# Performance work log

Hardware: AMD Instinct MI355X
Metric: run time of the kernel (lower is better)

Reference implementation:

```python
import jax, jax.numpy as jnp
import numpy as np

B, S, D, VOCAB = 8, 32, 256, 50257
N = 4 * 64          # n_devices * neurons_per_device
K = max(N // 5, 8)  # top-k active neurons = 51


def _make_edges():
    # mimics the torch init loop: 4*N random (src,dst) draws, keep src!=dst, dedup, preserve order
    rng = np.random.default_rng(0)
    s = rng.integers(0, N, 4 * N)
    d = rng.integers(0, N, 4 * N)
    seen, es, ed = set(), [], []
    for a, b in zip(s.tolist(), d.tolist()):
        if a != b and (a, b) not in seen:
            seen.add((a, b)); es.append(a); ed.append(b)
    return np.asarray(es, np.int32), np.asarray(ed, np.int32)


def setup_inputs() -> dict:
    key = jax.random.key(0)
    ks = jax.random.split(key, 12)
    es, ed = _make_edges()
    E = es.shape[0]
    f32 = jnp.float32
    return {
        "input_ids": jax.random.randint(ks[0], (B, S), 0, VOCAB),
        "embed":     jax.random.normal(ks[1], (VOCAB, D), f32) * 0.02,
        "pos_embed": jax.random.normal(ks[2], (S, D), f32) * 0.02,
        "router_W":  jax.random.normal(ks[3], (N, D), f32) * 0.02,
        "router_b":  jnp.zeros((N,), f32),
        "fc_W":      jax.random.normal(ks[4], (N, D, D), f32) * 0.02,
        "fc_b":      jnp.zeros((N, D), f32),
        "gate_W":    jax.random.normal(ks[5], (N, D), f32) * 0.02,
        "gate_b":    jnp.zeros((N,), f32),
        "conn_W":    jax.random.normal(ks[6], (E, D, D), f32) * 0.02,
        "ln_g":      jnp.ones((D,), f32),
        "ln_b":      jnp.zeros((D,), f32),
        "out_W":     jax.random.normal(ks[7], (VOCAB, D), f32) * 0.02,
        "out_b":     jnp.zeros((VOCAB,), f32),
        "edge_src":  jnp.asarray(es),
        "edge_dst":  jnp.asarray(ed),
    }


def _forward(input_ids, embed, pos_embed, router_W, router_b, fc_W, fc_b,
             gate_W, gate_b, conn_W, ln_g, ln_b, out_W, out_b, edge_src, edge_dst):
    x = embed[input_ids] + pos_embed[None, :, :]  # [B,S,D]

    def propagate(xt):  # xt: [B,D] -> [B,D]
        scores = xt @ router_W.T + router_b                  # [B,N]
        vals, idx = jax.lax.top_k(scores, K)                 # [B,K]
        active = idx[0]                                      # batch-elem-0 picks the active set (as in torch code)
        w = jax.nn.softmax(vals, axis=-1)                    # [B,K]
        # hop 0: active neurons applied to routed input
        h = jnp.einsum('bd,kod->kbo', xt, fc_W[active]) + fc_b[active][:, None, :]
        g = jax.nn.sigmoid(jnp.einsum('bd,kd->kb', xt, gate_W[active]) + gate_b[active][:, None])
        states = jax.nn.gelu(h, approximate=False) * g[:, :, None] * w.T[:, :, None]  # [K,B,D]
        # edge pass: only edges with both endpoints active contribute
        member = jnp.zeros((N,), bool).at[active].set(True)
        pos = jnp.zeros((N,), jnp.int32).at[active].set(jnp.arange(K, dtype=jnp.int32))
        emask = (member[edge_src] & member[edge_dst]).astype(xt.dtype)               # [E]
        sig = jnp.einsum('ebd,eod->ebo', states[pos[edge_src]], conn_W)              # [E,B,D]
        hh = jnp.einsum('ebd,eod->ebo', sig, fc_W[edge_dst]) + fc_b[edge_dst][:, None, :]
        gg = jax.nn.sigmoid(jnp.einsum('ebd,ed->eb', sig, gate_W[edge_dst]) + gate_b[edge_dst][:, None])
        act = jax.nn.gelu(hh, approximate=False) * gg[:, :, None] * emask[:, None, None]
        nxt = jax.ops.segment_sum(act, pos[edge_dst], num_segments=K)                # [K,B,D]
        return (states + 0.5 * nxt).mean(axis=0)                                     # [B,D]

    out = jax.vmap(propagate, in_axes=1, out_axes=1)(x)      # [B,S,D]
    mu = out.mean(-1, keepdims=True)
    var = ((out - mu) ** 2).mean(-1, keepdims=True)
    out = (out - mu) * jax.lax.rsqrt(var + 1e-5) * ln_g + ln_b
    return out @ out_W.T + out_b                             # [B,S,VOCAB]


def reference(input_ids, embed, pos_embed, router_W, router_b, fc_W, fc_b,
              gate_W, gate_b, conn_W, ln_g, ln_b, out_W, out_b, edge_src, edge_dst):
    return _forward(input_ids, embed, pos_embed, router_W, router_b, fc_W, fc_b,
                    gate_W, gate_b, conn_W, ln_g, ln_b, out_W, out_b, edge_src, edge_dst)
```

## Files before the change

kernel.cpp:

```cpp
#include <hip/hip_runtime.h>
#include <math.h>

#define B_ 8
#define S_ 32
#define D_ 256
#define N_ 256
#define K_ 51
#define V_ 50257

__device__ __forceinline__ float dot4f(float4 a, float4 b){
  return a.x*b.x + a.y*b.y + a.z*b.z + a.w*b.w;
}
__device__ __forceinline__ float gelu_exact(float x){
  return 0.5f * x * (1.0f + erff(x * 0.70710678118654752440f));
}
__device__ __forceinline__ float sigmoidf_(float x){
  return 1.0f / (1.0f + expf(-x));
}

__global__ __launch_bounds__(256) void k_embed(const int* __restrict__ ids,
    const float* __restrict__ embed, const float* __restrict__ pose,
    float* __restrict__ xt)
{
  int bx = blockIdx.x;
  int t = bx >> 3, b = bx & 7;
  int d = threadIdx.x;
  int id = ids[b * S_ + t];
  xt[(size_t)bx * D_ + d] = embed[(size_t)id * D_ + d] + pose[(size_t)t * D_ + d];
}

__global__ __launch_bounds__(256) void k_router(const float* __restrict__ xt,
    const float* __restrict__ rW, const float* __restrict__ rb,
    float* __restrict__ scores)
{
  int bx = blockIdx.x;
  int tid = threadIdx.x;
  __shared__ float4 xs4[64];
  if (tid < 64) xs4[tid] = ((const float4*)(xt + (size_t)bx * D_))[tid];
  __syncthreads();
  float acc = rb[tid];
  const float4* wp = (const float4*)(rW + (size_t)tid * D_);
  for (int d4 = 0; d4 < 64; d4++){
    float4 w = wp[d4]; float4 x = xs4[d4];
    acc += dot4f(w, x);
  }
  scores[(size_t)bx * N_ + tid] = acc;
}

__global__ __launch_bounds__(256) void k_topk(const float* __restrict__ scores,
    float* __restrict__ wbuf, int* __restrict__ active,
    int* __restrict__ member, int* __restrict__ pos)
{
  int bx = blockIdx.x;
  int t = bx >> 3, b = bx & 7;
  int tid = threadIdx.x;
  __shared__ float sv[256];
  __shared__ int   si[256];
  __shared__ float ex[K_];
  __shared__ float exsum;
  sv[tid] = scores[(size_t)bx * N_ + tid];
  si[tid] = tid;
  for (int kk = 2; kk <= 256; kk <<= 1){
    for (int j = kk >> 1; j > 0; j >>= 1){
      __syncthreads();
      int ixj = tid ^ j;
      if (ixj > tid){
        float va = sv[tid], vb = sv[ixj];
        int   ia = si[tid], ib = si[ixj];
        bool before = (va > vb) || (va == vb && ia < ib);
        bool up = ((tid & kk) == 0);
        if (up != before){
          sv[tid] = vb; sv[ixj] = va;
          si[tid] = ib; si[ixj] = ia;
        }
      }
    }
  }
  __syncthreads();
  float vmax = sv[0];
  if (tid < K_) ex[tid] = expf(sv[tid] - vmax);
  __syncthreads();
  if (tid == 0){
    float s = 0.0f;
    for (int k = 0; k < K_; k++) s += ex[k];
    exsum = s;
  }
  __syncthreads();
  if (tid < K_) wbuf[(size_t)bx * K_ + tid] = ex[tid] / exsum;
  if (b == 0){
    member[t * N_ + tid] = 0;
    pos[t * N_ + tid] = 0;
    __syncthreads();
    if (tid < K_){
      int nn = si[tid];
      active[t * K_ + tid] = nn;
      member[t * N_ + nn] = 1;
      pos[t * N_ + nn] = tid;
    }
  }
}

__global__ __launch_bounds__(256) void k_chunks(const int* __restrict__ esrc,
    const int* __restrict__ edst, const int* __restrict__ member,
    int E, int* __restrict__ ccount, unsigned int* __restrict__ chunks)
{
  int e = blockIdx.x * 256 + threadIdx.x;
  if (e >= E) return;
  int src = esrc[e], dst = edst[e];
  unsigned int mask = 0;
  for (int t = 0; t < S_; t++)
    if (member[t * N_ + src] && member[t * N_ + dst]) mask |= (1u << t);
  while (mask){
    int t0 = __ffs(mask) - 1; mask &= mask - 1;
    unsigned int t1 = 0xFFu;
    if (mask){ t1 = (unsigned int)(__ffs(mask) - 1); mask &= mask - 1; }
    int ci = atomicAdd(ccount, 1);
    chunks[ci] = (unsigned int)e | ((unsigned int)t0 << 16) | (t1 << 24);
  }
}

__global__ __launch_bounds__(256) void k_hop0(const float* __restrict__ xt,
    const float* __restrict__ fcW, const float* __restrict__ fcB,
    const float* __restrict__ gateW, const float* __restrict__ gateB,
    const float* __restrict__ wbuf, const int* __restrict__ active,
    float* __restrict__ states)
{
  int k = blockIdx.x, t = blockIdx.y;
  int tid = threadIdx.x;
  __shared__ float xs[B_ * D_];
  __shared__ float gl[B_];
  __shared__ float wl[B_];
  int n = active[t * K_ + k];
  float4* xs4 = (float4*)xs;
  const float4* xt4 = (const float4*)(xt + (size_t)t * B_ * D_);
  #pragma unroll
  for (int i = 0; i < 2; i++) xs4[tid + i * 256] = xt4[tid + i * 256];
  if (tid < B_) wl[tid] = wbuf[(size_t)(t * B_ + tid) * K_ + k];
  __syncthreads();
  {
    int wave = tid >> 6, lane = tid & 63;
    float4 gw = ((const float4*)(gateW + (size_t)n * D_))[lane];
    float a0 = dot4f(gw, xs4[(wave * 2 + 0) * 64 + lane]);
    float a1 = dot4f(gw, xs4[(wave * 2 + 1) * 64 + lane]);
    for (int s2 = 1; s2 < 64; s2 <<= 1){
      a0 += __shfl_xor(a0, s2, 64);
      a1 += __shfl_xor(a1, s2, 64);
    }
    if (lane == 0){
      float gb = gateB[n];
      gl[wave * 2 + 0] = sigmoidf_(a0 + gb);
      gl[wave * 2 + 1] = sigmoidf_(a1 + gb);
    }
  }
  __syncthreads();
  float acc[B_] = {0,0,0,0,0,0,0,0};
  const float4* wp = (const float4*)(fcW + (size_t)n * D_ * D_ + (size_t)tid * D_);
  for (int d4 = 0; d4 < 64; d4++){
    float4 w = wp[d4];
    #pragma unroll
    for (int b = 0; b < B_; b++) acc[b] += dot4f(w, xs4[b * 64 + d4]);
  }
  float fb = fcB[(size_t)n * D_ + tid];
  #pragma unroll
  for (int b = 0; b < B_; b++){
    float s = gelu_exact(acc[b] + fb) * gl[b] * wl[b];
    states[((size_t)(t * K_ + k) * B_ + b) * D_ + tid] = s;
  }
}

__global__ __launch_bounds__(256) void k_edge3(const float* __restrict__ states,
    const float* __restrict__ connW, const float* __restrict__ fcW,
    const float* __restrict__ fcB, const float* __restrict__ gateW,
    const float* __restrict__ gateB, const int* __restrict__ esrc,
    const int* __restrict__ edst, const int* __restrict__ pos,
    const int* __restrict__ ccount, const unsigned int* __restrict__ chunks,
    float* __restrict__ nxt)
{
  __shared__ float xs[2 * B_ * D_];
  __shared__ float sg[2 * B_ * D_];
  __shared__ float gl[16];
  int nch = *ccount;
  int tid = threadIdx.x;
  float4* xs4 = (float4*)xs;
  float4* sg4 = (float4*)sg;
  for (int it = blockIdx.x; it < nch; it += gridDim.x){
    unsigned int pk = chunks[it];
    int e  = (int)(pk & 0xFFFFu);
    int t0 = (int)((pk >> 16) & 0xFFu);
    int t1 = (int)((pk >> 24) & 0xFFu);
    int nc = (t1 == 0xFF) ? 1 : 2;
    int src = esrc[e], dst = edst[e];
    int ks0 = pos[t0 * N_ + src], kd0 = pos[t0 * N_ + dst];
    {
      const float4* s0 = (const float4*)(states + (size_t)(t0 * K_ + ks0) * B_ * D_);
      xs4[tid] = s0[tid]; xs4[tid + 256] = s0[tid + 256];
      if (nc == 2){
        int ks1 = pos[t1 * N_ + src];
        const float4* s1 = (const float4*)(states + (size_t)(t1 * K_ + ks1) * B_ * D_);
        xs4[tid + 512] = s1[tid]; xs4[tid + 768] = s1[tid + 256];
      }
    }
    __syncthreads();
    {
      const float4* wp = (const float4*)(connW + (size_t)e * D_ * D_ + (size_t)tid * D_);
      if (nc == 2){
        float a0[B_] = {0,0,0,0,0,0,0,0};
        float a1[B_] = {0,0,0,0,0,0,0,0};
        #pragma unroll 16
        for (int d4 = 0; d4 < 64; d4++){
          float4 w = wp[d4];
          #pragma unroll
          for (int b = 0; b < B_; b++){
            a0[b] += dot4f(w, xs4[b * 64 + d4]);
            a1[b] += dot4f(w, xs4[512 + b * 64 + d4]);
          }
        }
        #pragma unroll
        for (int b = 0; b < B_; b++){
          sg[b * D_ + tid] = a0[b];
          sg[2048 + b * D_ + tid] = a1[b];
        }
      } else {
        float a0[B_] = {0,0,0,0,0,0,0,0};
        #pragma unroll 16
        for (int d4 = 0; d4 < 64; d4++){
          float4 w = wp[d4];
          #pragma unroll
          for (int b = 0; b < B_; b++) a0[b] += dot4f(w, xs4[b * 64 + d4]);
        }
        #pragma unroll
        for (int b = 0; b < B_; b++) sg[b * D_ + tid] = a0[b];
      }
    }
    __syncthreads();
    {
      int wv = tid >> 6, ln = tid & 63;
      float4 gw = ((const float4*)(gateW + (size_t)dst * D_))[ln];
      float gb = gateB[dst];
      for (int p = wv; p < 8 * nc; p += 4){
        float a = dot4f(gw, sg4[(p >> 3) * 512 + (p & 7) * 64 + ln]);
        for (int s2 = 1; s2 < 64; s2 <<= 1) a += __shfl_xor(a, s2, 64);
        if (ln == 0) gl[p] = sigmoidf_(a + gb);
      }
    }
    __syncthreads();
    {
      const float4* wq = (const float4*)(fcW + (size_t)dst * D_ * D_ + (size_t)tid * D_);
      float fb = fcB[(size_t)dst * D_ + tid];
      if (nc == 2){
        float b0[B_] = {0,0,0,0,0,0,0,0};
        float b1[B_] = {0,0,0,0,0,0,0,0};
        #pragma unroll 16
        for (int d4 = 0; d4 < 64; d4++){
          float4 w = wq[d4];
          #pragma unroll
          for (int b = 0; b < B_; b++){
            b0[b] += dot4f(w, sg4[b * 64 + d4]);
            b1[b] += dot4f(w, sg4[512 + b * 64 + d4]);
          }
        }
        int kd1 = pos[t1 * N_ + dst];
        float* nx0 = nxt + (size_t)(t0 * K_ + kd0) * B_ * D_;
        float* nx1 = nxt + (size_t)(t1 * K_ + kd1) * B_ * D_;
        #pragma unroll
        for (int b = 0; b < B_; b++){
          atomicAdd(&nx0[b * D_ + tid], gelu_exact(b0[b] + fb) * gl[b]);
          atomicAdd(&nx1[b * D_ + tid], gelu_exact(b1[b] + fb) * gl[8 + b]);
        }
      } else {
        float b0[B_] = {0,0,0,0,0,0,0,0};
        #pragma unroll 16
        for (int d4 = 0; d4 < 64; d4++){
          float4 w = wq[d4];
          #pragma unroll
          for (int b = 0; b < B_; b++) b0[b] += dot4f(w, sg4[b * 64 + d4]);
        }
        float* nx0 = nxt + (size_t)(t0 * K_ + kd0) * B_ * D_;
        #pragma unroll
        for (int b = 0; b < B_; b++)
          atomicAdd(&nx0[b * D_ + tid], gelu_exact(b0[b] + fb) * gl[b]);
      }
    }
    __syncthreads();
  }
}

__global__ __launch_bounds__(256) void k_ln(const float* __restrict__ states,
    const float* __restrict__ nxt, const float* __restrict__ lng,
    const float* __restrict__ lnb, float* __restrict__ normed)
{
  int row = blockIdx.x;
  int b = row >> 5, t = row & 31;
  int d = threadIdx.x;
  float v = 0.0f;
  for (int k = 0; k < K_; k++){
    size_t idx = ((size_t)(t * K_ + k) * B_ + b) * D_ + d;
    v += states[idx] + 0.5f * nxt[idx];
  }
  v /= 51.0f;
  __shared__ float red[256];
  red[d] = v; __syncthreads();
  for (int s = 128; s > 0; s >>= 1){ if (d < s) red[d] += red[d + s]; __syncthreads(); }
  float mu = red[0] * (1.0f / 256.0f);
  __syncthreads();
  float c = v - mu;
  red[d] = c * c; __syncthreads();
  for (int s = 128; s > 0; s >>= 1){ if (d < s) red[d] += red[d + s]; __syncthreads(); }
  float var = red[0] * (1.0f / 256.0f);
  normed[(size_t)row * D_ + d] = c * rsqrtf(var + 1e-5f) * lng[d] + lnb[d];
}

__global__ __launch_bounds__(256) void k_logits(const float* __restrict__ normed,
    const float* __restrict__ outW, const float* __restrict__ outB,
    float* __restrict__ out)
{
  __shared__ float Ws[64][132];
  __shared__ float Xs[64][68];
  int tid = threadIdx.x;
  int vbase = blockIdx.x * 128;
  int rbase = blockIdx.y * 64;
  int cg = tid & 31;
  int rg = tid >> 5;
  float acc[8][4];
  #pragma unroll
  for (int i = 0; i < 8; i++)
    #pragma unroll
    for (int j = 0; j < 4; j++) acc[i][j] = 0.0f;

  for (int kb = 0; kb < 4; kb++){
    if (kb) __syncthreads();
    #pragma unroll
    for (int i = 0; i < 8; i++){
      int idx = tid + i * 256;
      int v = idx >> 4, kq = idx & 15;
      int gv = vbase + v;
      float4 w = make_float4(0.0f, 0.0f, 0.0f, 0.0f);
      if (gv < V_) w = ((const float4*)(outW + (size_t)gv * D_))[kb * 16 + kq];
      Ws[kq * 4 + 0][v] = w.x;
      Ws[kq * 4 + 1][v] = w.y;
      Ws[kq * 4 + 2][v] = w.z;
      Ws[kq * 4 + 3][v] = w.w;
    }
    #pragma unroll
    for (int i = 0; i < 4; i++){
      int idx = tid + i * 256;
      int r = idx >> 4, kq = idx & 15;
      float4 x = ((const float4*)(normed + (size_t)(rbase + r) * D_))[kb * 16 + kq];
      Xs[kq * 4 + 0][r] = x.x;
      Xs[kq * 4 + 1][r] = x.y;
      Xs[kq * 4 + 2][r] = x.z;
      Xs[kq * 4 + 3][r] = x.w;
    }
    __syncthreads();
    #pragma unroll 4
    for (int k = 0; k < 64; k++){
      float4 wv = *(const float4*)&Ws[k][cg * 4];
      float4 x0 = *(const float4*)&Xs[k][rg * 8];
      float4 x1 = *(const float4*)&Xs[k][rg * 8 + 4];
      float xr[8] = {x0.x, x0.y, x0.z, x0.w, x1.x, x1.y, x1.z, x1.w};
      float wc[4] = {wv.x, wv.y, wv.z, wv.w};
      #pragma unroll
      for (int i = 0; i < 8; i++)
        #pragma unroll
        for (int j = 0; j < 4; j++)
          acc[i][j] = fmaf(xr[i], wc[j], acc[i][j]);
    }
  }
  #pragma unroll
  for (int j = 0; j < 4; j++){
    int gc = vbase + cg * 4 + j;
    if (gc < V_){
      float ob = outB[gc];
      #pragma unroll
      for (int i = 0; i < 8; i++)
        out[(size_t)(rbase + rg * 8 + i) * V_ + gc] = acc[i][j] + ob;
    }
  }
}

extern "C" void kernel_launch(void* const* d_in, const int* in_sizes, int n_in,
                              void* d_out, int out_size, void* d_ws, size_t ws_size,
                              hipStream_t stream)
{
  const int*   ids    = (const int*)d_in[0];
  const float* embed  = (const float*)d_in[1];
  const float* pose   = (const float*)d_in[2];
  const float* rW     = (const float*)d_in[3];
  const float* rb     = (const float*)d_in[4];
  const float* fcW    = (const float*)d_in[5];
  const float* fcB    = (const float*)d_in[6];
  const float* gateW  = (const float*)d_in[7];
  const float* gateB  = (const float*)d_in[8];
  const float* connW  = (const float*)d_in[9];
  const float* lng    = (const float*)d_in[10];
  const float* lnb    = (const float*)d_in[11];
  const float* outW   = (const float*)d_in[12];
  const float* outB   = (const float*)d_in[13];
  const int*   esrc   = (const int*)d_in[14];
  const int*   edst   = (const int*)d_in[15];
  int E = in_sizes[14];
  float* out = (float*)d_out;

  char* ws = (char*)d_ws;
  float* xt     = (float*)(ws + 0);
  float* scores = (float*)(ws + 262144);
  unsigned int* chunks = (unsigned int*)(ws + 262144);
  float* wbuf   = (float*)(ws + 524288);
  int*   active = (int*)  (ws + 589824);
  int*   ccount = (int*)  (ws + 596992);
  int*   member = (int*)  (ws + 598016);
  int*   pos    = (int*)  (ws + 630784);
  float* states = (float*)(ws + 663552);
  float* nxt    = (float*)(ws + 14032896);
  float* normed = (float*)(ws + 27402240);

  hipMemsetAsync(nxt, 0, (size_t)3342336 * 4, stream);

  k_embed  <<<dim3(S_ * B_), 256, 0, stream>>>(ids, embed, pose, xt);
  k_router <<<dim3(S_ * B_), 256, 0, stream>>>(xt, rW, rb, scores);
  k_topk   <<<dim3(S_ * B_), 256, 0, stream>>>(scores, wbuf, active, member, pos);
  hipMemsetAsync(ccount, 0, 4, stream);
  k_chunks <<<dim3((E + 255) / 256), 256, 0, stream>>>(esrc, edst, member, E, ccount, chunks);
  k_hop0   <<<dim3(K_, S_), 256, 0, stream>>>(xt, fcW, fcB, gateW, gateB, wbuf, active, states);
  k_edge3  <<<dim3(1024), 256, 0, stream>>>(states, connW, fcW, fcB, gateW, gateB,
                                            esrc, edst, pos, ccount, chunks, nxt);
  k_ln     <<<dim3(B_ * S_), 256, 0, stream>>>(states, nxt, lng, lnb, normed);
  k_logits <<<dim3((V_ + 127) / 128, 4), 256, 0, stream>>>(normed, outW, outB, out);
}
```

Baseline: 795.8 us.

## Group hop0 by neuron across timesteps and tile edge matmuls through shared memory

Hop0 is reorganised so each block handles one neuron for up to four timesteps. The neuron's fc weight is loaded once and reused via a shared-memory-tiled register-blocked GEMM, and the block also zeroes the matching nxt slices, which replaces the big memset. The edge kernel switches from per-thread full-row weight reads to cooperatively staged, transposed weight tiles in shared memory with a 4x4 register-blocked outer product. This cuts redundant global weight traffic and improves coalescing, at the cost of more syncs, more shared memory and an extra small chunk-building kernel.

```diff
diff --git a/kernel.cpp b/kernel.cpp
--- a/kernel.cpp
+++ b/kernel.cpp
@@ -119,52 +119,121 @@
   }
 }
 
+__global__ __launch_bounds__(256) void k_nchunks(const int* __restrict__ member,
+    int* __restrict__ ncount, unsigned int* __restrict__ nchunks)
+{
+  int n = threadIdx.x;
+  unsigned int mask = 0;
+  for (int t = 0; t < S_; t++)
+    if (member[t * N_ + n]) mask |= (1u << t);
+  while (mask){
+    unsigned int t0 = (unsigned int)(__ffs(mask) - 1); mask &= mask - 1;
+    unsigned int t1 = 0x3Fu, t2 = 0x3Fu, t3 = 0x3Fu;
+    if (mask){ t1 = (unsigned int)(__ffs(mask) - 1); mask &= mask - 1; }
+    if (mask){ t2 = (unsigned int)(__ffs(mask) - 1); mask &= mask - 1; }
+    if (mask){ t3 = (unsigned int)(__ffs(mask) - 1); mask &= mask - 1; }
+    int ci = atomicAdd(ncount, 1);
+    nchunks[ci] = (unsigned int)n | (t0 << 8) | (t1 << 14) | (t2 << 20) | (t3 << 26);
+  }
+}
+
 __global__ __launch_bounds__(256) void k_hop0(const float* __restrict__ xt,
     const float* __restrict__ fcW, const float* __restrict__ fcB,
     const float* __restrict__ gateW, const float* __restrict__ gateB,
-    const float* __restrict__ wbuf, const int* __restrict__ active,
-    float* __restrict__ states)
-{
-  int k = blockIdx.x, t = blockIdx.y;
+    const float* __restrict__ wbuf, const int* __restrict__ pos,
+    const int* __restrict__ ncount, const unsigned int* __restrict__ nchunks,
+    float* __restrict__ states, float* __restrict__ nxt)
+{
+  __shared__ float XT[256][36];
+  __shared__ float Ws[32][260];
+  __shared__ float gl[32];
+  int nch = *ncount;
   int tid = threadIdx.x;
-  __shared__ float xs[B_ * D_];
-  __shared__ float gl[B_];
-  __shared__ float wl[B_];
-  int n = active[t * K_ + k];
-  float4* xs4 = (float4*)xs;
-  const float4* xt4 = (const float4*)(xt + (size_t)t * B_ * D_);
-  #pragma unroll
-  for (int i = 0; i < 2; i++) xs4[tid + i * 256] = xt4[tid + i * 256];
-  if (tid < B_) wl[tid] = wbuf[(size_t)(t * B_ + tid) * K_ + k];
-  __syncthreads();
-  {
-    int wave = tid >> 6, lane = tid & 63;
-    float4 gw = ((const float4*)(gateW + (size_t)n * D_))[lane];
-    float a0 = dot4f(gw, xs4[(wave * 2 + 0) * 64 + lane]);
-    float a1 = dot4f(gw, xs4[(wave * 2 + 1) * 64 + lane]);
-    for (int s2 = 1; s2 < 64; s2 <<= 1){
-      a0 += __shfl_xor(a0, s2, 64);
-      a1 += __shfl_xor(a1, s2, 64);
-    }
-    if (lane == 0){
+  int cg = tid & 63;
+  int rg = tid >> 6;
+  for (int it = blockIdx.x; it < nch; it += gridDim.x){
+    __syncthreads();
+    unsigned int pk = nchunks[it];
+    int n = (int)(pk & 255u);
+    int nt = 1 + (((pk >> 14) & 63u) != 63u) + (((pk >> 20) & 63u) != 63u)
+               + (((pk >> 26) & 63u) != 63u);
+    #pragma unroll
+    for (int i = 0; i < 8; i++){
+      int idx = tid + i * 256;
+      int r = idx & 31, kq = idx >> 5;
+      int ti = r >> 3, b = r & 7;
+      float4 v = make_float4(0.0f, 0.0f, 0.0f, 0.0f);
+      if (ti < nt){
+        int t = (int)((pk >> (8 + 6 * ti)) & 63u);
+        v = ((const float4*)(xt + (size_t)(t * 8 + b) * D_))[kq];
+      }
+      XT[kq * 4 + 0][r] = v.x;
+      XT[kq * 4 + 1][r] = v.y;
+      XT[kq * 4 + 2][r] = v.z;
+      XT[kq * 4 + 3][r] = v.w;
+    }
+    if (rg < nt){
+      int t = (int)((pk >> (8 + 6 * rg)) & 63u);
+      float4 gw = ((const float4*)(gateW + (size_t)n * D_))[cg];
       float gb = gateB[n];
-      gl[wave * 2 + 0] = sigmoidf_(a0 + gb);
-      gl[wave * 2 + 1] = sigmoidf_(a1 + gb);
-    }
-  }
-  __syncthreads();
-  float acc[B_] = {0,0,0,0,0,0,0,0};
-  const float4* wp = (const float4*)(fcW + (size_t)n * D_ * D_ + (size_t)tid * D_);
-  for (int d4 = 0; d4 < 64; d4++){
-    float4 w = wp[d4];
-    #pragma unroll
-    for (int b = 0; b < B_; b++) acc[b] += dot4f(w, xs4[b * 64 + d4]);
-  }
-  float fb = fcB[(size_t)n * D_ + tid];
-  #pragma unroll
-  for (int b = 0; b < B_; b++){
-    float s = gelu_exact(acc[b] + fb) * gl[b] * wl[b];
-    states[((size_t)(t * K_ + k) * B_ + b) * D_ + tid] = s;
+      for (int b = 0; b < 8; b++){
+        float a = dot4f(gw, ((const float4*)(xt + (size_t)(t * 8 + b) * D_))[cg]);
+        for (int s2 = 1; s2 < 64; s2 <<= 1) a += __shfl_xor(a, s2, 64);
+        if (cg == 0) gl[rg * 8 + b] = sigmoidf_(a + gb);
+      }
+    }
+    __syncthreads();
+    float acc[8][4];
+    #pragma unroll
+    for (int i = 0; i < 8; i++)
+      #pragma unroll
+      for (int j = 0; j < 4; j++) acc[i][j] = 0.0f;
+    const float4* wsrc = (const float4*)(fcW + (size_t)n * D_ * D_);
+    for (int kb = 0; kb < 8; kb++){
+      if (kb) __syncthreads();
+      #pragma unroll
+      for (int i = 0; i < 8; i++){
+        int idx = tid + i * 256;
+        int o = idx >> 3, q = idx & 7;
+        float4 w = wsrc[(size_t)o * 64 + kb * 8 + q];
+        Ws[q * 4 + 0][o] = w.x;
+        Ws[q * 4 + 1][o] = w.y;
+        Ws[q * 4 + 2][o] = w.z;
+        Ws[q * 4 + 3][o] = w.w;
+      }
+      __syncthreads();
+      #pragma unroll 8
+      for (int kk = 0; kk < 32; kk++){
+        float4 w = *(const float4*)&Ws[kk][cg * 4];
+        float4 xa = *(const float4*)&XT[kb * 32 + kk][rg * 8];
+        float4 xb = *(const float4*)&XT[kb * 32 + kk][rg * 8 + 4];
+        float xr[8] = {xa.x, xa.y, xa.z, xa.w, xb.x, xb.y, xb.z, xb.w};
+        float wc[4] = {w.x, w.y, w.z, w.w};
+        #pragma unroll
+        for (int i = 0; i < 8; i++)
+          #pragma unroll
+          for (int j = 0; j < 4; j++)
+            acc[i][j] = fmaf(xr[i], wc[j], acc[i][j]);
+      }
+    }
+    if (rg < nt){
+      int t = (int)((pk >> (8 + 6 * rg)) & 63u);
+      int kpos = pos[t * N_ + n];
+      float4 fb = ((const float4*)(fcB + (size_t)n * D_))[cg];
+      #pragma unroll
+      for (int b = 0; b < 8; b++){
+        float w_ = wbuf[(size_t)(t * 8 + b) * K_ + kpos];
+        float g_ = gl[rg * 8 + b];
+        float4 o4;
+        o4.x = gelu_exact(acc[b][0] + fb.x) * g_ * w_;
+        o4.y = gelu_exact(acc[b][1] + fb.y) * g_ * w_;
+        o4.z = gelu_exact(acc[b][2] + fb.z) * g_ * w_;
+        o4.w = gelu_exact(acc[b][3] + fb.w) * g_ * w_;
+        size_t base = ((size_t)(t * K_ + kpos) * 8 + b) * D_ + cg * 4;
+        *(float4*)(states + base) = o4;
+        *(float4*)(nxt + base) = make_float4(0.0f, 0.0f, 0.0f, 0.0f);
+      }
+    }
   }
 }
 
@@ -176,14 +245,16 @@
     const int* __restrict__ ccount, const unsigned int* __restrict__ chunks,
     float* __restrict__ nxt)
 {
-  __shared__ float xs[2 * B_ * D_];
-  __shared__ float sg[2 * B_ * D_];
+  __shared__ float XT[256][20];
+  __shared__ float Ws[32][260];
+  __shared__ float sgl[16][260];
   __shared__ float gl[16];
   int nch = *ccount;
   int tid = threadIdx.x;
-  float4* xs4 = (float4*)xs;
-  float4* sg4 = (float4*)sg;
+  int cg = tid & 63;
+  int rg = tid >> 6;
   for (int it = blockIdx.x; it < nch; it += gridDim.x){
+    __syncthreads();
     unsigned int pk = chunks[it];
     int e  = (int)(pk & 0xFFFFu);
     int t0 = (int)((pk >> 16) & 0xFFu);
@@ -191,97 +262,132 @@
     int nc = (t1 == 0xFF) ? 1 : 2;
     int src = esrc[e], dst = edst[e];
     int ks0 = pos[t0 * N_ + src], kd0 = pos[t0 * N_ + dst];
+    int ks1 = (nc == 2) ? pos[t1 * N_ + src] : 0;
+    int kd1 = (nc == 2) ? pos[t1 * N_ + dst] : 0;
+    #pragma unroll
+    for (int i = 0; i < 4; i++){
+      int idx = tid + i * 256;
+      int r = idx & 15, kq = idx >> 4;
+      int c = r >> 3, b = r & 7;
+      float4 v = make_float4(0.0f, 0.0f, 0.0f, 0.0f);
+      if (c < nc){
+        int t = c ? t1 : t0;
+        int ks = c ? ks1 : ks0;
+        v = ((const float4*)(states + ((size_t)(t * K_ + ks) * 8 + b) * D_))[kq];
+      }
+      XT[kq * 4 + 0][r] = v.x;
+      XT[kq * 4 + 1][r] = v.y;
+      XT[kq * 4 + 2][r] = v.z;
+      XT[kq * 4 + 3][r] = v.w;
+    }
+    __syncthreads();
+    float acc[4][4];
+    #pragma unroll
+    for (int i = 0; i < 4; i++)
+      #pragma unroll
+      for (int j = 0; j < 4; j++) acc[i][j] = 0.0f;
     {
-      const float4* s0 = (const float4*)(states + (size_t)(t0 * K_ + ks0) * B_ * D_);
-      xs4[tid] = s0[tid]; xs4[tid + 256] = s0[tid + 256];
-      if (nc == 2){
-        int ks1 = pos[t1 * N_ + src];
-        const float4* s1 = (const float4*)(states + (size_t)(t1 * K_ + ks1) * B_ * D_);
-        xs4[tid + 512] = s1[tid]; xs4[tid + 768] = s1[tid + 256];
-      }
-    }
-    __syncthreads();
+      const float4* wsrc = (const float4*)(connW + (size_t)e * D_ * D_);
+      for (int kb = 0; kb < 8; kb++){
+        if (kb) __syncthreads();
+        #pragma unroll
+        for (int i = 0; i < 8; i++){
+          int idx = tid + i * 256;
+          int o = idx >> 3, q = idx & 7;
+          float4 w = wsrc[(size_t)o * 64 + kb * 8 + q];
+          Ws[q * 4 + 0][o] = w.x;
+          Ws[q * 4 + 1][o] = w.y;
+          Ws[q * 4 + 2][o] = w.z;
+          Ws[q * 4 + 3][o] = w.w;
+        }
+        __syncthreads();
+        #pragma unroll 8
+        for (int kk = 0; kk < 32; kk++){
+          float4 w = *(const float4*)&Ws[kk][cg * 4];
+          float4 x = *(const float4*)&XT[kb * 32 + kk][rg * 4];
+          float xr[4] = {x.x, x.y, x.z, x.w};
+          float wc[4] = {w.x, w.y, w.z, w.w};
+          #pragma unroll
+          for (int i = 0; i < 4; i++)
+            #pragma unroll
+            for (int j = 0; j < 4; j++)
+              acc[i][j] = fmaf(xr[i], wc[j], acc[i][j]);
+        }
+      }
+    }
+    #pragma unroll
+    for (int i = 0; i < 4; i++)
+      *(float4*)&sgl[rg * 4 + i][cg * 4] = make_float4(acc[i][0], acc[i][1], acc[i][2], acc[i][3]);
+    __syncthreads();
+    #pragma unroll
+    for (int i = 0; i < 4; i++){
+      int idx = tid + i * 256;
+      int r = idx & 15, kq = idx >> 4;
+      float4 v = *(const float4*)&sgl[r][kq * 4];
+      XT[kq * 4 + 0][r] = v.x;
+      XT[kq * 4 + 1][r] = v.y;
+      XT[kq * 4 + 2][r] = v.z;
+      XT[kq * 4 + 3][r] = v.w;
+    }
     {
-      const float4* wp = (const float4*)(connW + (size_t)e * D_ * D_ + (size_t)tid * D_);
-      if (nc == 2){
-        float a0[B_] = {0,0,0,0,0,0,0,0};
-        float a1[B_] = {0,0,0,0,0,0,0,0};
-        #pragma unroll 16
-        for (int d4 = 0; d4 < 64; d4++){
-          float4 w = wp[d4];
+      float4 gw = ((const float4*)(gateW + (size_t)dst * D_))[cg];
+      float gb = gateB[dst];
+      for (int p = rg; p < 8 * nc; p += 4){
+        float a = dot4f(gw, *(const float4*)&sgl[p][cg * 4]);
+        for (int s2 = 1; s2 < 64; s2 <<= 1) a += __shfl_xor(a, s2, 64);
+        if (cg == 0) gl[p] = sigmoidf_(a + gb);
+      }
+    }
+    __syncthreads();
+    #pragma unroll
+    for (int i = 0; i < 4; i++)
+      #pragma unroll
+      for (int j = 0; j < 4; j++) acc[i][j] = 0.0f;
+    {
+      const float4* wsrc = (const float4*)(fcW + (size_t)dst * D_ * D_);
+      for (int kb = 0; kb < 8; kb++){
+        if (kb) __syncthreads();
+        #pragma unroll
+        for (int i = 0; i < 8; i++){
+          int idx = tid + i * 256;
+          int o = idx >> 3, q = idx & 7;
+          float4 w = wsrc[(size_t)o * 64 + kb * 8 + q];
+          Ws[q * 4 + 0][o] = w.x;
+          Ws[q * 4 + 1][o] = w.y;
+          Ws[q * 4 + 2][o] = w.z;
+          Ws[q * 4 + 3][o] = w.w;
+        }
+        __syncthreads();
+        #pragma unroll 8
+        for (int kk = 0; kk < 32; kk++){
+          float4 w = *(const float4*)&Ws[kk][cg * 4];
+          float4 x = *(const float4*)&XT[kb * 32 + kk][rg * 4];
+          float xr[4] = {x.x, x.y, x.z, x.w};
+          float wc[4] = {w.x, w.y, w.z, w.w};
           #pragma unroll
-          for (int b = 0; b < B_; b++){
-            a0[b] += dot4f(w, xs4[b * 64 + d4]);
-            a1[b] += dot4f(w, xs4[512 + b * 64 + d4]);
-          }
+          for (int i = 0; i < 4; i++)
+            #pragma unroll
+            for (int j = 0; j < 4; j++)
+              acc[i][j] = fmaf(xr[i], wc[j], acc[i][j]);
         }
-        #pragma unroll
-        for (int b = 0; b < B_; b++){
-          sg[b * D_ + tid] = a0[b];
-          sg[2048 + b * D_ + tid] = a1[b];
-        }
-      } else {
-        float a0[B_] = {0,0,0,0,0,0,0,0};
-        #pragma unroll 16
-        for (int d4 = 0; d4 < 64; d4++){
-          float4 w = wp[d4];
-          #pragma unroll
-          for (int b = 0; b < B_; b++) a0[b] += dot4f(w, xs4[b * 64 + d4]);
-        }
-        #pragma unroll
-        for (int b = 0; b < B_; b++) sg[b * D_ + tid] = a0[b];
-      }
-    }
-    __syncthreads();
-    {
-      int wv = tid >> 6, ln = tid & 63;
-      float4 gw = ((const float4*)(gateW + (size_t)dst * D_))[ln];
-      float gb = gateB[dst];
-      for (int p = wv; p < 8 * nc; p += 4){
-        float a = dot4f(gw, sg4[(p >> 3) * 512 + (p & 7) * 64 + ln]);
-        for (int s2 = 1; s2 < 64; s2 <<= 1) a += __shfl_xor(a, s2, 64);
-        if (ln == 0) gl[p] = sigmoidf_(a + gb);
-      }
-    }
-    __syncthreads();
-    {
-      const float4* wq = (const float4*)(fcW + (size_t)dst * D_ * D_ + (size_t)tid * D_);
-      float fb = fcB[(size_t)dst * D_ + tid];
-      if (nc == 2){
-        float b0[B_] = {0,0,0,0,0,0,0,0};
-        float b1[B_] = {0,0,0,0,0,0,0,0};
-        #pragma unroll 16
-        for (int d4 = 0; d4 < 64; d4++){
-          float4 w = wq[d4];
-          #pragma unroll
-          for (int b = 0; b < B_; b++){
-            b0[b] += dot4f(w, sg4[b * 64 + d4]);
-            b1[b] += dot4f(w, sg4[512 + b * 64 + d4]);
-          }
-        }
-        int kd1 = pos[t1 * N_ + dst];
-        float* nx0 = nxt + (size_t)(t0 * K_ + kd0) * B_ * D_;
-        float* nx1 = nxt + (size_t)(t1 * K_ + kd1) * B_ * D_;
-        #pragma unroll
-        for (int b = 0; b < B_; b++){
-          atomicAdd(&nx0[b * D_ + tid], gelu_exact(b0[b] + fb) * gl[b]);
-          atomicAdd(&nx1[b * D_ + tid], gelu_exact(b1[b] + fb) * gl[8 + b]);
-        }
-      } else {
-        float b0[B_] = {0,0,0,0,0,0,0,0};
-        #pragma unroll 16
-        for (int d4 = 0; d4 < 64; d4++){
-          float4 w = wq[d4];
-          #pragma unroll
-          for (int b = 0; b < B_; b++) b0[b] += dot4f(w, sg4[b * 64 + d4]);
-        }
-        float* nx0 = nxt + (size_t)(t0 * K_ + kd0) * B_ * D_;
-        #pragma unroll
-        for (int b = 0; b < B_; b++)
-          atomicAdd(&nx0[b * D_ + tid], gelu_exact(b0[b] + fb) * gl[b]);
-      }
-    }
-    __syncthreads();
+      }
+    }
+    float4 fb = ((const float4*)(fcB + (size_t)dst * D_))[cg];
+    #pragma unroll
+    for (int i = 0; i < 4; i++){
+      int m = rg * 4 + i;
+      int c = m >> 3, b = m & 7;
+      if (c < nc){
+        int t = c ? t1 : t0;
+        int kd = c ? kd1 : kd0;
+        float g_ = gl[m];
+        float* nx = nxt + ((size_t)(t * K_ + kd) * 8 + b) * D_ + cg * 4;
+        atomicAdd(&nx[0], gelu_exact(acc[i][0] + fb.x) * g_);
+        atomicAdd(&nx[1], gelu_exact(acc[i][1] + fb.y) * g_);
+        atomicAdd(&nx[2], gelu_exact(acc[i][2] + fb.z) * g_);
+        atomicAdd(&nx[3], gelu_exact(acc[i][3] + fb.w) * g_);
+      }
+    }
   }
 }
 
@@ -404,24 +510,26 @@
   char* ws = (char*)d_ws;
   float* xt     = (float*)(ws + 0);
   float* scores = (float*)(ws + 262144);
-  unsigned int* chunks = (unsigned int*)(ws + 262144);
+  unsigned int* chunks  = (unsigned int*)(ws + 262144);
+  unsigned int* nchunks = (unsigned int*)(ws + 327680);
   float* wbuf   = (float*)(ws + 524288);
   int*   active = (int*)  (ws + 589824);
   int*   ccount = (int*)  (ws + 596992);
+  int*   ncount = (int*)  (ws + 596996);
   int*   member = (int*)  (ws + 598016);
   int*   pos    = (int*)  (ws + 630784);
   float* states = (float*)(ws + 663552);
   float* nxt    = (float*)(ws + 14032896);
   float* normed = (float*)(ws + 27402240);
 
-  hipMemsetAsync(nxt, 0, (size_t)3342336 * 4, stream);
-
   k_embed  <<<dim3(S_ * B_), 256, 0, stream>>>(ids, embed, pose, xt);
   k_router <<<dim3(S_ * B_), 256, 0, stream>>>(xt, rW, rb, scores);
   k_topk   <<<dim3(S_ * B_), 256, 0, stream>>>(scores, wbuf, active, member, pos);
-  hipMemsetAsync(ccount, 0, 4, stream);
+  hipMemsetAsync(ccount, 0, 8, stream);
   k_chunks <<<dim3((E + 255) / 256), 256, 0, stream>>>(esrc, edst, member, E, ccount, chunks);
-  k_hop0   <<<dim3(K_, S_), 256, 0, stream>>>(xt, fcW, fcB, gateW, gateB, wbuf, active, states);
+  k_nchunks<<<dim3(1), 256, 0, stream>>>(member, ncount, nchunks);
+  k_hop0   <<<dim3(512), 256, 0, stream>>>(xt, fcW, fcB, gateW, gateB, wbuf, pos,
+                                           ncount, nchunks, states, nxt);
   k_edge3  <<<dim3(1024), 256, 0, stream>>>(states, connW, fcW, fcB, gateW, gateB,
                                             esrc, edst, pos, ccount, chunks, nxt);
   k_ln     <<<dim3(B_ * S_), 256, 0, stream>>>(states, nxt, lng, lnb, normed);
```

New measurement: 709.6 us. 1.12x faster.
